# Kernel optimization log

Hardware: AMD Instinct MI355X
Metric: run time of the kernel (lower is better)

The kernel has to match this reference:

```python
import jax, jax.numpy as jnp
import numpy as np
import math

HEADS = 16
DIMS = 1024
SEQ_LEN = 2048
RANK_K = 128
BATCH = 8


def setup_inputs() -> dict:
    key = jax.random.key(0)
    ks = jax.random.split(key, 14)
    dh_std = 1.0 / math.sqrt(DIMS)
    proj_std = 1.0 / math.sqrt(RANK_K)
    inp = {
        "q": jax.random.normal(ks[0], (BATCH, SEQ_LEN, DIMS), jnp.float32),
        "k": jax.random.normal(ks[1], (BATCH, SEQ_LEN, DIMS), jnp.float32),
        "v": jax.random.normal(ks[2], (BATCH, SEQ_LEN, DIMS), jnp.float32),
        # nn.Linear weights [out, in], bias [out]
        "Wq": jax.random.uniform(ks[3], (DIMS, DIMS), jnp.float32, -dh_std, dh_std),
        "bq": jax.random.uniform(ks[4], (DIMS,), jnp.float32, -dh_std, dh_std),
        "Wk": jax.random.uniform(ks[5], (DIMS, DIMS), jnp.float32, -dh_std, dh_std),
        "bk": jax.random.uniform(ks[6], (DIMS,), jnp.float32, -dh_std, dh_std),
        "Wv": jax.random.uniform(ks[7], (DIMS, DIMS), jnp.float32, -dh_std, dh_std),
        "bv": jax.random.uniform(ks[8], (DIMS,), jnp.float32, -dh_std, dh_std),
        # Linformer low-rank projections [seq_length, k], uniform(-1/sqrt(k), 1/sqrt(k))
        "proj_k": jax.random.uniform(ks[9], (SEQ_LEN, RANK_K), jnp.float32, -proj_std, proj_std),
        "proj_v": jax.random.uniform(ks[10], (SEQ_LEN, RANK_K), jnp.float32, -proj_std, proj_std),
        "Wo": jax.random.uniform(ks[11], (DIMS, DIMS), jnp.float32, -dh_std, dh_std),
        "bo": jax.random.uniform(ks[12], (DIMS,), jnp.float32, -dh_std, dh_std),
    }
    return inp


def reference(q, k, v, Wq, bq, Wk, bk, Wv, bv, proj_k, proj_v, Wo, bo):
    B, N, D = q.shape
    H = HEADS
    dh = D // H
    Kr = proj_k.shape[1]

    kp = k @ Wk.T + bk                       # [B, N, D]
    # faithful to original: plain reshape (view), NOT a head-split transpose
    qp = (q @ Wq.T + bq).reshape(B, H, N, dh)  # [B, H, N, dh]
    vp = v @ Wv.T + bv                       # [B, N, D]

    pk = jnp.einsum('bnd,nk->bkd', kp, proj_k[:N])  # [B, Kr, D]
    pv = jnp.einsum('bnd,nk->bkd', vp, proj_v[:N])  # [B, Kr, D]
    pk = pk.reshape(B, Kr, H, dh).transpose(0, 2, 1, 3)  # [B, H, Kr, dh]
    pv = pv.reshape(B, Kr, H, dh).transpose(0, 2, 1, 3)  # [B, H, Kr, dh]

    # scores [B,H,N,Kr] -> transposed to [B,H,Kr,N]; softmax over N (seq) axis
    scores = jnp.einsum('bhnd,bhkd->bhkn', qp, pk) / math.sqrt(dh)
    attn = jax.nn.softmax(scores, axis=-1)   # [B, H, Kr, N]
    out = jnp.einsum('bhkn,bhkd->bhnd', attn, pv)  # [B, H, N, dh]
    out = out.transpose(0, 2, 1, 3).reshape(B, N, D)
    return out @ Wo.T + bo
```

## Files before the change

kernel.cpp:

```cpp
#include <hip/hip_runtime.h>

typedef unsigned short u16;
typedef unsigned int   u32;
typedef __attribute__((ext_vector_type(4))) float fx4;
typedef __attribute__((ext_vector_type(8))) __bf16 bf16x8;
typedef __attribute__((ext_vector_type(4))) __bf16 bf16x4;
typedef __attribute__((ext_vector_type(8))) unsigned short us8;
typedef __attribute__((ext_vector_type(2))) unsigned int u32x2;

__device__ __forceinline__ u16 f2bf(float x){
  u32 u = __builtin_bit_cast(u32, x);
  u += 0x7fffu + ((u >> 16) & 1u);
  return (u16)(u >> 16);
}
__device__ __forceinline__ float b2f(u16 h){
  u32 u = ((u32)h) << 16;
  return __builtin_bit_cast(float, u);
}
__device__ __forceinline__ void gld16(const void* g, void* l){
  __builtin_amdgcn_global_load_lds(
      (const __attribute__((address_space(1))) u32*)g,
      (__attribute__((address_space(3))) u32*)l, 16, 0, 0);
}
__device__ __forceinline__ void xcd_remap(u32& bx, u32& by, u32& bz){
  u32 nx = gridDim.x, ny = gridDim.y, nz = gridDim.z;
  u32 nwg = nx * ny * nz;
  u32 orig = (blockIdx.z * ny + blockIdx.y) * nx + blockIdx.x;
  u32 lid = (orig & 7u) * (nwg >> 3) + (orig >> 3);
  bx = lid % nx;
  u32 rem = lid / nx;
  by = rem % ny;
  bz = rem / ny;
}

__global__ __launch_bounds__(256) void k_f2bfAll(const float* __restrict__ w0,
                                                 const float* __restrict__ w1,
                                                 const float* __restrict__ w2,
                                                 const float* __restrict__ w3,
                                                 const float* __restrict__ q,
                                                 u16* __restrict__ wout,
                                                 u16* __restrict__ qout,
                                                 float* __restrict__ zbuf){
  if (blockIdx.x == 0 && blockIdx.y == 0) zbuf[threadIdx.x] = 0.f;
  const int y = blockIdx.y;
  const float* src;
  u16* dst;
  if (y < 4){
    src = y == 0 ? w0 : y == 1 ? w1 : y == 2 ? w2 : w3;
    dst = wout + (long)y * 1048576;
  } else {
    src = q + (long)(y - 4) * 1048576;
    dst = qout + (long)(y - 4) * 1048576;
  }
  int i = blockIdx.x * 256 + threadIdx.x;
  const int stride = gridDim.x * 256;
  for (; i < 131072; i += stride){
    const float4* p = (const float4*)src + (long)i * 2;
    float4 a = p[0], b = p[1];
    us8 o = { f2bf(a.x), f2bf(a.y), f2bf(a.z), f2bf(a.w),
              f2bf(b.x), f2bf(b.y), f2bf(b.z), f2bf(b.w) };
    *((us8*)dst + i) = o;
  }
}

__global__ __launch_bounds__(256) void k_tconvP(const float* __restrict__ pjk,
                                                const float* __restrict__ pjv,
                                                u16* __restrict__ projT,
                                                float* __restrict__ ssum){
  const int z = blockIdx.z;
  const float* in = z ? pjv : pjk;
  u16* out = projT + z * 262144;
  float* colsum = ssum + z * 128;
  const int c0 = blockIdx.x * 64, r0 = blockIdx.y * 64;
  __shared__ u16 tile[64][66];
  __shared__ float red[256];
  const int t = threadIdx.x;
  const int cc = t & 63, wq = t >> 6;
  float part = 0.f;
  #pragma unroll
  for (int i = 0; i < 16; ++i){
    int rr = i * 4 + wq;
    float v = in[(long)(r0 + rr) * 128 + c0 + cc];
    tile[rr][cc] = f2bf(v);
    part += v;
  }
  red[t] = part;
  __syncthreads();
  if (t < 64){
    float s = red[t] + red[t + 64] + red[t + 128] + red[t + 192];
    atomicAdd(&colsum[c0 + t], s);
  }
  __syncthreads();
  const int oc0 = t >> 5, jb = (t & 31) * 2;
  #pragma unroll
  for (int i = 0; i < 8; ++i){
    int oc = oc0 + i * 8;
    u32 pk2 = (u32)tile[jb][oc] | ((u32)tile[jb + 1][oc] << 16);
    *(u32*)(out + (long)(c0 + oc) * 2048 + r0 + jb) = pk2;
  }
}

__global__ __launch_bounds__(256) void k_gemmTN(
    const u16* __restrict__ projT, const float* __restrict__ ksrc,
    const float* __restrict__ vsrc, u16* __restrict__ ck)
{
  u32 bx, by, bz; xcd_remap(bx, by, bz);
  const int p = bz >> 3, b = bz & 7;
  const u16* A = projT + p * 262144 + by * 64 * 2048;
  const float* S = (p ? vsrc : ksrc) + (long)b * 2097152;
  u16* C = ck + p * 1048576 + b * 131072 + by * 65536;
  const int d0 = bx * 64;
  __shared__ u16 ldsA[3][64 * 64];
  __shared__ u16 ldsB[3][64 * 72];
  const int t = threadIdx.x, lane = t & 63, w = t >> 6;
  const int wm = w >> 1, wn = w & 1;
  const int r15 = lane & 15, g = lane >> 4;
  const int c4 = t & 15, r4 = t >> 4;

  auto ldA = [&](int kt, int buf){
    #pragma unroll
    for (int i = 0; i < 2; ++i){
      int ch = i * 256 + t, row = ch >> 3, cc = ch & 7;
      gld16(A + (long)row * 2048 + kt + ((cc ^ (row & 7)) * 8),
            (char*)ldsA[buf] + ch * 16);
    }
  };
  auto ldS = [&](int kt, float4* f){
    #pragma unroll
    for (int i = 0; i < 4; ++i)
      f[i] = *(const float4*)(S + (long)(kt + r4 * 4 + i) * 1024 + d0 + c4 * 4);
  };
  auto wrB = [&](const float4* f, int buf){
    #pragma unroll
    for (int j = 0; j < 4; ++j){
      const int d = c4 * 4 + j;
      u32 lo = (u32)f2bf(((const float*)&f[0])[j]) | ((u32)f2bf(((const float*)&f[1])[j]) << 16);
      u32 hi = (u32)f2bf(((const float*)&f[2])[j]) | ((u32)f2bf(((const float*)&f[3])[j]) << 16);
      u32x2 pr = { lo, hi };
      *(u32x2*)&ldsB[buf][d * 72 + ((r4 ^ (d & 15)) * 4)] = pr;
    }
  };

  fx4 acc[2][2] = {};
  auto compute = [&](int buf){
    #pragma unroll
    for (int ks = 0; ks < 2; ++ks){
      bf16x8 af[2], bfv[2];
      #pragma unroll
      for (int mf = 0; mf < 2; ++mf){
        int row = wm * 32 + mf * 16 + r15;
        af[mf] = *(const bf16x8*)((const char*)ldsA[buf] + row * 128 +
                                  (((ks * 4 + g) ^ (row & 7)) * 16));
      }
      #pragma unroll
      for (int nf = 0; nf < 2; ++nf){
        const int d = wn * 32 + nf * 16 + r15, x = d & 15;
        const int q0 = ks * 8 + g * 2;
        bf16x4 lo = *(const bf16x4*)&ldsB[buf][d * 72 + ((q0 ^ x) * 4)];
        bf16x4 hi = *(const bf16x4*)&ldsB[buf][d * 72 + (((q0 + 1) ^ x) * 4)];
        bfv[nf] = __builtin_shufflevector(lo, hi, 0, 1, 2, 3, 4, 5, 6, 7);
      }
      #pragma unroll
      for (int mf = 0; mf < 2; ++mf)
        #pragma unroll
        for (int nf = 0; nf < 2; ++nf)
          acc[mf][nf] = __builtin_amdgcn_mfma_f32_16x16x32_bf16(af[mf], bfv[nf], acc[mf][nf], 0, 0, 0);
    }
  };

  float4 fa[4], fb[4];
  ldS(0, fa); ldA(0, 0);
  ldS(64, fb); ldA(64, 1);
  asm volatile("s_waitcnt vmcnt(6)" ::: "memory");
  wrB(fa, 0);
  asm volatile("s_waitcnt lgkmcnt(0)" ::: "memory");
  __builtin_amdgcn_s_barrier();
  asm volatile("" ::: "memory");

  for (int tt = 0; tt < 32; tt += 2){
    {
      const bool pf = (tt + 2 < 32);
      if (pf){ ldS((tt + 2) * 64, fa); ldA((tt + 2) * 64, (tt + 2) % 3); }
      asm volatile("" ::: "memory");
      compute(tt % 3);
      if (pf) { asm volatile("s_waitcnt vmcnt(6)" ::: "memory"); }
      else    { asm volatile("s_waitcnt vmcnt(0)" ::: "memory"); }
      wrB(fb, (tt + 1) % 3);
      asm volatile("s_waitcnt lgkmcnt(0)" ::: "memory");
      __builtin_amdgcn_s_barrier();
      asm volatile("" ::: "memory");
    }
    {
      const bool pf = (tt + 3 < 32);
      const bool hv = (tt + 2 < 32);
      if (pf){ ldS((tt + 3) * 64, fb); ldA((tt + 3) * 64, (tt + 3) % 3); }
      asm volatile("" ::: "memory");
      compute((tt + 1) % 3);
      if (hv){
        if (pf) { asm volatile("s_waitcnt vmcnt(6)" ::: "memory"); }
        else    { asm volatile("s_waitcnt vmcnt(0)" ::: "memory"); }
        wrB(fa, (tt + 2) % 3);
      }
      asm volatile("s_waitcnt lgkmcnt(0)" ::: "memory");
      __builtin_amdgcn_s_barrier();
      asm volatile("" ::: "memory");
    }
  }

  #pragma unroll
  for (int mf = 0; mf < 2; ++mf)
    #pragma unroll
    for (int nf = 0; nf < 2; ++nf){
      const int row0 = wm * 32 + mf * 16 + g * 4;
      const int col  = d0 + wn * 32 + nf * 16 + r15;
      #pragma unroll
      for (int r = 0; r < 4; ++r)
        C[(long)(row0 + r) * 1024 + col] = f2bf(acc[mf][nf][r]);
    }
}

__global__ __launch_bounds__(256) void k_pkpv(
    const u16* __restrict__ ck, const u16* __restrict__ Wk_bf,
    const u16* __restrict__ Wv_bf, const float* __restrict__ bk,
    const float* __restrict__ bv, const float* __restrict__ ssum,
    u16* __restrict__ pk, u16* __restrict__ pvT)
{
  constexpr int BM = 64, BN = 64, BK = 64;
  __shared__ u16 ldsA[BM * BK];
  __shared__ u16 ldsB[BN * BK];
  u32 bx, by, bz;
  xcd_remap(bx, by, bz);
  const int half = bz >> 3, b = bz & 7;
  const u16* A = ck + half * 1048576 + b * 131072;
  const u16* B = half ? Wv_bf : Wk_bf;
  const float* bias = half ? bv : bk;
  const float* srow = ssum + half * 128;
  const float scale = half ? 1.f : 0.125f;
  const int t = threadIdx.x;
  const int lane = t & 63;
  const int w = t >> 6, wm = w >> 1, wn = w & 1;
  const int r15 = lane & 15, g = lane >> 4;
  const int m0 = by * BM, n0 = bx * BN;
  fx4 acc[2][2] = {};
  for (int kt = 0; kt < 1024; kt += BK){
    #pragma unroll
    for (int i = 0; i < 2; ++i){
      int ch = i * 256 + t, row = ch >> 3, cc = ch & 7;
      gld16(A + (long)(m0 + row) * 1024 + kt + cc * 8, (char*)ldsA + ch * 16);
    }
    #pragma unroll
    for (int i = 0; i < 2; ++i){
      int ch = i * 256 + t, row = ch >> 3, cc = ch & 7;
      gld16(B + (long)(n0 + row) * 1024 + kt + cc * 8, (char*)ldsB + ch * 16);
    }
    __syncthreads();
    #pragma unroll
    for (int ks = 0; ks < 2; ++ks){
      bf16x8 af[2], bfv[2];
      #pragma unroll
      for (int mf = 0; mf < 2; ++mf)
        af[mf] = *(const bf16x8*)&ldsA[(wm * 32 + mf * 16 + r15) * BK + ks * 32 + g * 8];
      #pragma unroll
      for (int nf = 0; nf < 2; ++nf)
        bfv[nf] = *(const bf16x8*)&ldsB[(wn * 32 + nf * 16 + r15) * BK + ks * 32 + g * 8];
      #pragma unroll
      for (int mf = 0; mf < 2; ++mf)
        #pragma unroll
        for (int nf = 0; nf < 2; ++nf)
          acc[mf][nf] = __builtin_amdgcn_mfma_f32_16x16x32_bf16(af[mf], bfv[nf], acc[mf][nf], 0, 0, 0);
    }
    __syncthreads();
  }
  #pragma unroll
  for (int mf = 0; mf < 2; ++mf){
    #pragma unroll
    for (int nf = 0; nf < 2; ++nf){
      const int row0 = m0 + wm * 32 + mf * 16 + g * 4;
      const int col  = n0 + wn * 32 + nf * 16 + r15;
      float vv[4];
      #pragma unroll
      for (int r = 0; r < 4; ++r)
        vv[r] = (acc[mf][nf][r] + srow[row0 + r] * bias[col]) * scale;
      if (!half){
        #pragma unroll
        for (int r = 0; r < 4; ++r)
          pk[b * 131072 + (long)(row0 + r) * 1024 + col] = f2bf(vv[r]);
      } else {
        u32 lo = (u32)f2bf(vv[0]) | ((u32)f2bf(vv[1]) << 16);
        u32 hi = (u32)f2bf(vv[2]) | ((u32)f2bf(vv[3]) << 16);
        u32x2 pk2 = { lo, hi };
        *(u32x2*)(pvT + b * 131072 + (long)col * 128 + row0) = pk2;
      }
    }
  }
}

template<int EPI, typename OutT>
__global__ __launch_bounds__(512, 1) void k_gemm256b(
    const u16* __restrict__ A, int lda,
    const u16* __restrict__ B, int ldb,
    OutT* __restrict__ C, int ldc,
    int K, const float* __restrict__ bias)
{
  constexpr int BM = 256, BN = 256, BK = 64;
  __shared__ u16 ldsA[2][BM * BK];
  __shared__ u16 ldsB[2][BN * BK];
  u32 bx, by, bz;
  xcd_remap(bx, by, bz);
  const int m0 = by * BM, n0 = bx * BN;
  const int t = threadIdx.x, lane = t & 63, w = t >> 6;
  const int wm = w >> 2, wn = w & 3;
  const int r15 = lane & 15, g = lane >> 4;
  const int NT = K >> 6;

  auto stA = [&](int buf, int half, int kt){
    #pragma unroll
    for (int j = 0; j < 2; ++j){
      int ch = j * 512 + t, row = ch >> 3, cc = ch & 7;
      gld16(A + (long)(m0 + half * 128 + row) * lda + kt + ((cc ^ (row & 7)) * 8),
            (char*)ldsA[buf] + half * 16384 + ch * 16);
    }
  };
  auto stB = [&](int buf, int half, int kt){
    #pragma unroll
    for (int j = 0; j < 2; ++j){
      int ch = j * 512 + t, row = ch >> 3, cc = ch & 7;
      gld16(B + (long)(n0 + half * 128 + row) * ldb + kt + ((cc ^ (row & 7)) * 8),
            (char*)ldsB[buf] + half * 16384 + ch * 16);
    }
  };

  stB(0,0,0); stB(0,1,0); stA(0,0,0); stA(0,1,0);
  if (NT > 1){ stB(1,0,BK); stB(1,1,BK); stA(1,0,BK); }
  asm volatile("s_waitcnt vmcnt(6)" ::: "memory");
  __builtin_amdgcn_s_barrier();
  asm volatile("" ::: "memory");

  fx4 acc[8][4] = {};
  for (int tt = 0; tt < NT; ++tt){
    const int buf = tt & 1;
    bf16x8 a[2][4], b01[2][2], b23[2][2];
    #pragma unroll
    for (int ks = 0; ks < 2; ++ks)
      #pragma unroll
      for (int mf = 0; mf < 4; ++mf){
        int row = wm * 128 + mf * 16 + r15;
        a[ks][mf] = *(const bf16x8*)((const char*)ldsA[buf] + row * 128 + (((ks*4+g) ^ (r15 & 7)) * 16));
      }
    #pragma unroll
    for (int ks = 0; ks < 2; ++ks)
      #pragma unroll
      for (int nf = 0; nf < 2; ++nf){
        int row = wn * 64 + nf * 16 + r15;
        b01[ks][nf] = *(const bf16x8*)((const char*)ldsB[buf] + row * 128 + (((ks*4+g) ^ (r15 & 7)) * 16));
      }
    if (tt + 1 < NT) stA(buf ^ 1, 1, (tt + 1) * BK);
    __builtin_amdgcn_s_setprio(1);
    #pragma unroll
    for (int ks = 0; ks < 2; ++ks)
      #pragma unroll
      for (int mf = 0; mf < 4; ++mf)
        #pragma unroll
        for (int nf = 0; nf < 2; ++nf)
          acc[mf][nf] = __builtin_amdgcn_mfma_f32_16x16x32_bf16(a[ks][mf], b01[ks][nf], acc[mf][nf], 0, 0, 0);
    __builtin_amdgcn_s_setprio(0);
    asm volatile("" ::: "memory");
    __builtin_amdgcn_s_barrier();
    asm volatile("" ::: "memory");
    #pragma unroll
    for (int ks = 0; ks < 2; ++ks)
      #pragma unroll
      for (int nf = 0; nf < 2; ++nf){
        int row = wn * 64 + (nf + 2) * 16 + r15;
        b23[ks][nf] = *(const bf16x8*)((const char*)ldsB[buf] + row * 128 + (((ks*4+g) ^ (r15 & 7)) * 16));
      }
    __builtin_amdgcn_s_setprio(1);
    #pragma unroll
    for (int ks = 0; ks < 2; ++ks)
      #pragma unroll
      for (int mf = 0; mf < 4; ++mf)
        #pragma unroll
        for (int nf = 0; nf < 2; ++nf)
          acc[mf][nf + 2] = __builtin_amdgcn_mfma_f32_16x16x32_bf16(a[ks][mf], b23[ks][nf], acc[mf][nf + 2], 0, 0, 0);
    __builtin_amdgcn_s_setprio(0);
    asm volatile("" ::: "memory");
    __builtin_amdgcn_s_barrier();
    asm volatile("" ::: "memory");
    #pragma unroll
    for (int ks = 0; ks < 2; ++ks)
      #pragma unroll
      for (int mf = 0; mf < 4; ++mf){
        int row = wm * 128 + (mf + 4) * 16 + r15;
        a[ks][mf] = *(const bf16x8*)((const char*)ldsA[buf] + row * 128 + (((ks*4+g) ^ (r15 & 7)) * 16));
      }
    if (tt + 2 < NT) stB(buf, 0, (tt + 2) * BK);
    __builtin_amdgcn_s_setprio(1);
    #pragma unroll
    for (int ks = 0; ks < 2; ++ks)
      #pragma unroll
      for (int mf = 0; mf < 4; ++mf)
        #pragma unroll
        for (int nf = 0; nf < 2; ++nf)
          acc[mf + 4][nf + 2] = __builtin_amdgcn_mfma_f32_16x16x32_bf16(a[ks][mf], b23[ks][nf], acc[mf + 4][nf + 2], 0, 0, 0);
    __builtin_amdgcn_s_setprio(0);
    asm volatile("" ::: "memory");
    __builtin_amdgcn_s_barrier();
    asm volatile("" ::: "memory");
    if (tt + 2 < NT){ stA(buf, 0, (tt + 2) * BK); stB(buf, 1, (tt + 2) * BK); }
    __builtin_amdgcn_s_setprio(1);
    #pragma unroll
    for (int ks = 0; ks < 2; ++ks)
      #pragma unroll
      for (int mf = 0; mf < 4; ++mf)
        #pragma unroll
        for (int nf = 0; nf < 2; ++nf)
          acc[mf + 4][nf] = __builtin_amdgcn_mfma_f32_16x16x32_bf16(a[ks][mf], b01[ks][nf], acc[mf + 4][nf], 0, 0, 0);
    __builtin_amdgcn_s_setprio(0);
    if (tt + 2 < NT)      { asm volatile("s_waitcnt vmcnt(6)" ::: "memory"); }
    else if (tt + 1 < NT) { asm volatile("s_waitcnt vmcnt(0)" ::: "memory"); }
    asm volatile("" ::: "memory");
    __builtin_amdgcn_s_barrier();
    asm volatile("" ::: "memory");
  }

  #pragma unroll
  for (int mf = 0; mf < 8; ++mf)
    #pragma unroll
    for (int nf = 0; nf < 4; ++nf){
      const int row0 = m0 + wm * 128 + mf * 16 + g * 4;
      const int col  = n0 + wn * 64 + nf * 16 + r15;
      float bcol = 0.f;
      if constexpr (EPI == 1) bcol = bias[col];
      #pragma unroll
      for (int r = 0; r < 4; ++r){
        float vv = acc[mf][nf][r] + bcol;
        if constexpr (sizeof(OutT) == 2) C[(long)(row0 + r) * ldc + col] = (OutT)f2bf(vv);
        else                             C[(long)(row0 + r) * ldc + col] = (OutT)vv;
      }
    }
}

__global__ __launch_bounds__(512) void k_stats(const u16* __restrict__ pk,
                                               const u16* __restrict__ qp,
                                               float* __restrict__ zpart){
  const int hf = blockIdx.x, z = blockIdx.y;
  const int b = z >> 4, h = z & 15;
  const u16* pkh = pk + b * 131072 + h * 64;
  const u16* qph = qp + (long)z * 131072;
  __shared__ u16 pkL[128 * 64];
  __shared__ float zred[8][128];
  const int t = threadIdx.x, lane = t & 63, w = t >> 6;
  const int r15 = lane & 15, g = lane >> 4;
  #pragma unroll
  for (int i = 0; i < 2; ++i){
    int ch = i * 512 + t, row = ch >> 3, cc = ch & 7;
    int csrc = cc ^ (row & 7);
    gld16(pkh + (long)row * 1024 + csrc * 8, (char*)pkL + ch * 16);
  }
  __syncthreads();
  float zacc[8][4] = {};
  for (int c = 0; c < 4; ++c){
    const int n0 = hf * 1024 + w * 128 + c * 32;
    fx4 acc[8][2] = {};
    #pragma unroll
    for (int ks = 0; ks < 2; ++ks){
      bf16x8 bq[2];
      #pragma unroll
      for (int nf = 0; nf < 2; ++nf)
        bq[nf] = *(const bf16x8*)(qph + (long)(n0 + nf * 16 + r15) * 64 + ks * 32 + g * 8);
      #pragma unroll
      for (int mf = 0; mf < 8; ++mf){
        int row = mf * 16 + r15;
        int x = (ks * 4 + g) ^ (row & 7);
        bf16x8 a = *(const bf16x8*)((const char*)pkL + row * 128 + x * 16);
        #pragma unroll
        for (int nf = 0; nf < 2; ++nf)
          acc[mf][nf] = __builtin_amdgcn_mfma_f32_16x16x32_bf16(a, bq[nf], acc[mf][nf], 0, 0, 0);
      }
    }
    #pragma unroll
    for (int mf = 0; mf < 8; ++mf)
      #pragma unroll
      for (int nf = 0; nf < 2; ++nf)
        #pragma unroll
        for (int r = 0; r < 4; ++r)
          zacc[mf][r] += __expf(acc[mf][nf][r]);
  }
  #pragma unroll
  for (int mf = 0; mf < 8; ++mf)
    #pragma unroll
    for (int r = 0; r < 4; ++r){
      float v = zacc[mf][r];
      v += __shfl_xor(v, 1); v += __shfl_xor(v, 2);
      v += __shfl_xor(v, 4); v += __shfl_xor(v, 8);
      zacc[mf][r] = v;
    }
  if (r15 == 0){
    #pragma unroll
    for (int mf = 0; mf < 8; ++mf)
      #pragma unroll
      for (int r = 0; r < 4; ++r)
        zred[w][mf * 16 + g * 4 + r] = zacc[mf][r];
  }
  __syncthreads();
  if (t < 128){
    float s = 0.f;
    #pragma unroll
    for (int w2 = 0; w2 < 8; ++w2) s += zred[w2][t];
    zpart[hf * 16384 + (long)z * 128 + t] = s;
  }
}

__global__ __launch_bounds__(256) void k_attn(const u16* __restrict__ pk,
                                              const u16* __restrict__ qp,
                                              const u16* __restrict__ pvT,
                                              const float* __restrict__ zpart,
                                              u16* __restrict__ outh){
  u32 bx, by, bz;
  xcd_remap(bx, by, bz);
  const int z = by, nb = bx;
  const int b = z >> 4, h = z & 15;
  const u16* pkh = pk  + b * 131072 + h * 64;
  const u16* qph = qp  + (long)z * 131072;
  const u16* pvh = pvT + b * 131072 + h * 8192;
  __shared__ u16 pkL[128 * 64];
  __shared__ u16 ptL[4][32 * 132];
  __shared__ float zL[128];
  const int t = threadIdx.x, lane = t & 63, w = t >> 6;
  const int r15 = lane & 15, g = lane >> 4;
  #pragma unroll
  for (int i = 0; i < 4; ++i){
    int ch = i * 256 + t, row = ch >> 3, cc = ch & 7;
    int csrc = cc ^ (row & 7);
    gld16(pkh + (long)row * 1024 + csrc * 8, (char*)pkL + ch * 16);
  }
  if (t < 128)
    zL[t] = 1.0f / (zpart[(long)z * 128 + t] + zpart[16384 + (long)z * 128 + t]);
  __syncthreads();
  const int n0 = nb * 128 + w * 32;
  fx4 acc[8][2] = {};
  #pragma unroll
  for (int ks = 0; ks < 2; ++ks){
    bf16x8 bq[2];
    #pragma unroll
    for (int nf = 0; nf < 2; ++nf)
      bq[nf] = *(const bf16x8*)(qph + (long)(n0 + nf * 16 + r15) * 64 + ks * 32 + g * 8);
    #pragma unroll
    for (int mf = 0; mf < 8; ++mf){
      int row = mf * 16 + r15;
      int x = (ks * 4 + g) ^ (row & 7);
      bf16x8 a = *(const bf16x8*)((const char*)pkL + row * 128 + x * 16);
      #pragma unroll
      for (int nf = 0; nf < 2; ++nf)
        acc[mf][nf] = __builtin_amdgcn_mfma_f32_16x16x32_bf16(a, bq[nf], acc[mf][nf], 0, 0, 0);
    }
  }
  u16* pt = ptL[w];
  #pragma unroll
  for (int mf = 0; mf < 8; ++mf){
    const int kb = mf * 16 + g * 4;
    const float z0 = zL[kb], z1 = zL[kb + 1], z2 = zL[kb + 2], z3 = zL[kb + 3];
    #pragma unroll
    for (int nf = 0; nf < 2; ++nf){
      const int nl = nf * 16 + r15;
      u32 lo = (u32)f2bf(__expf(acc[mf][nf][0]) * z0) |
               ((u32)f2bf(__expf(acc[mf][nf][1]) * z1) << 16);
      u32 hi = (u32)f2bf(__expf(acc[mf][nf][2]) * z2) |
               ((u32)f2bf(__expf(acc[mf][nf][3]) * z3) << 16);
      u32x2 pkd = { lo, hi };
      *(u32x2*)(pt + nl * 132 + kb) = pkd;
    }
  }
  fx4 o[2][4] = {};
  #pragma unroll
  for (int ks = 0; ks < 4; ++ks){
    bf16x8 bv[4];
    #pragma unroll
    for (int nf = 0; nf < 4; ++nf)
      bv[nf] = *(const bf16x8*)(pvh + (long)(nf * 16 + r15) * 128 + ks * 32 + g * 8);
    #pragma unroll
    for (int mf = 0; mf < 2; ++mf){
      bf16x8 pa = *(const bf16x8*)(pt + (mf * 16 + r15) * 132 + ks * 32 + g * 8);
      #pragma unroll
      for (int nf = 0; nf < 4; ++nf)
        o[mf][nf] = __builtin_amdgcn_mfma_f32_16x16x32_bf16(pa, bv[nf], o[mf][nf], 0, 0, 0);
    }
  }
  u16* og = outh + ((long)b * 2048 + n0) * 1024 + h * 64;
  #pragma unroll
  for (int mf = 0; mf < 2; ++mf)
    #pragma unroll
    for (int nf = 0; nf < 4; ++nf)
      #pragma unroll
      for (int r = 0; r < 4; ++r){
        int nl = mf * 16 + g * 4 + r;
        og[(long)nl * 1024 + nf * 16 + r15] = f2bf(o[mf][nf][r]);
      }
}

extern "C" void kernel_launch(void* const* d_in, const int* in_sizes, int n_in,
                              void* d_out, int out_size, void* d_ws, size_t ws_size,
                              hipStream_t stream)
{
  const float* q   = (const float*)d_in[0];
  const float* k   = (const float*)d_in[1];
  const float* v   = (const float*)d_in[2];
  const float* Wq  = (const float*)d_in[3];
  const float* bq  = (const float*)d_in[4];
  const float* Wk  = (const float*)d_in[5];
  const float* bk  = (const float*)d_in[6];
  const float* Wv  = (const float*)d_in[7];
  const float* bv  = (const float*)d_in[8];
  const float* pjk = (const float*)d_in[9];
  const float* pjv = (const float*)d_in[10];
  const float* Wo  = (const float*)d_in[11];
  const float* bo  = (const float*)d_in[12];

  if (ws_size < 152044544u) return;

  char* ws = (char*)d_ws;
  u16*  q_bf  = (u16*)(ws + 0);
  float* zpart = (float*)(ws + 33554432);
  u16*  W_bf  = (u16*)(ws + 100663296);
  u16*  projT = (u16*)(ws + 109051904);
  float* sk   = (float*)(ws + 110100480);
  u16*  qp    = (u16*)(ws + 110101504);
  u16*  ck    = (u16*)(ws + 143655936);
  u16*  pk    = (u16*)(ws + 147850240);
  u16*  pvT   = (u16*)(ws + 149947392);
  u16*  outh  = (u16*)(ws + 0);
  u16*  Wq_bf = W_bf, *Wk_bf = W_bf + 1048576, *Wv_bf = W_bf + 2097152, *Wo_bf = W_bf + 3145728;

  k_f2bfAll<<<dim3(128,20), 256, 0, stream>>>(Wq, Wk, Wv, Wo, q, W_bf, q_bf, sk);
  k_tconvP<<<dim3(2,32,2), 256, 0, stream>>>(pjk, pjv, projT, sk);

  k_gemm256b<1,u16><<<dim3(4,64), 512, 0, stream>>>(
      q_bf,1024, Wq_bf,1024, qp,1024, 1024, bq);
  k_gemmTN<<<dim3(16,2,16), 256, 0, stream>>>(projT, k, v, ck);
  k_pkpv<<<dim3(16,2,16), 256, 0, stream>>>(ck, Wk_bf, Wv_bf, bk, bv, sk, pk, pvT);
  k_stats<<<dim3(2,128), 512, 0, stream>>>(pk, qp, zpart);
  k_attn<<<dim3(16,128), 256, 0, stream>>>(pk, qp, pvT, zpart, outh);
  k_gemm256b<1,float><<<dim3(4,64), 512, 0, stream>>>(
      outh,1024, Wo_bf,1024, (float*)d_out,1024, 1024, bo);
}
```

Before: 221.7 us.

## Split gemmTN sequence reduction in two halves and sum partials in pkpv

Result: slower. 229.7 us (+3.6%).

```diff
diff --git a/kernel.cpp b/kernel.cpp
--- a/kernel.cpp
+++ b/kernel.cpp
@@ -102,13 +102,14 @@
 
 __global__ __launch_bounds__(256) void k_gemmTN(
     const u16* __restrict__ projT, const float* __restrict__ ksrc,
-    const float* __restrict__ vsrc, u16* __restrict__ ck)
+    const float* __restrict__ vsrc, u16* __restrict__ ckA,
+    u16* __restrict__ ckB)
 {
   u32 bx, by, bz; xcd_remap(bx, by, bz);
-  const int p = bz >> 3, b = bz & 7;
-  const u16* A = projT + p * 262144 + by * 64 * 2048;
-  const float* S = (p ? vsrc : ksrc) + (long)b * 2097152;
-  u16* C = ck + p * 1048576 + b * 131072 + by * 65536;
+  const int half = bz >> 4, p = (bz >> 3) & 1, b = bz & 7;
+  const u16* A = projT + p * 262144 + by * 64 * 2048 + half * 1024;
+  const float* S = (p ? vsrc : ksrc) + (long)b * 2097152 + (long)half * 1048576;
+  u16* C = (half ? ckB : ckA) + p * 1048576 + b * 131072 + by * 65536;
   const int d0 = bx * 64;
   __shared__ u16 ldsA[3][64 * 64];
   __shared__ u16 ldsB[3][64 * 72];
@@ -168,6 +169,7 @@
     }
   };
 
+  constexpr int NT = 16;
   float4 fa[4], fb[4];
   ldS(0, fa); ldA(0, 0);
   ldS(64, fb); ldA(64, 1);
@@ -177,9 +179,9 @@
   __builtin_amdgcn_s_barrier();
   asm volatile("" ::: "memory");
 
-  for (int tt = 0; tt < 32; tt += 2){
+  for (int tt = 0; tt < NT; tt += 2){
     {
-      const bool pf = (tt + 2 < 32);
+      const bool pf = (tt + 2 < NT);
       if (pf){ ldS((tt + 2) * 64, fa); ldA((tt + 2) * 64, (tt + 2) % 3); }
       asm volatile("" ::: "memory");
       compute(tt % 3);
@@ -191,8 +193,8 @@
       asm volatile("" ::: "memory");
     }
     {
-      const bool pf = (tt + 3 < 32);
-      const bool hv = (tt + 2 < 32);
+      const bool pf = (tt + 3 < NT);
+      const bool hv = (tt + 2 < NT);
       if (pf){ ldS((tt + 3) * 64, fb); ldA((tt + 3) * 64, (tt + 3) % 3); }
       asm volatile("" ::: "memory");
       compute((tt + 1) % 3);
@@ -220,9 +222,10 @@
 }
 
 __global__ __launch_bounds__(256) void k_pkpv(
-    const u16* __restrict__ ck, const u16* __restrict__ Wk_bf,
-    const u16* __restrict__ Wv_bf, const float* __restrict__ bk,
-    const float* __restrict__ bv, const float* __restrict__ ssum,
+    const u16* __restrict__ ckA, const u16* __restrict__ ckB,
+    const u16* __restrict__ Wk_bf, const u16* __restrict__ Wv_bf,
+    const float* __restrict__ bk, const float* __restrict__ bv,
+    const float* __restrict__ ssum,
     u16* __restrict__ pk, u16* __restrict__ pvT)
 {
   constexpr int BM = 64, BN = 64, BK = 64;
@@ -230,46 +233,50 @@
   __shared__ u16 ldsB[BN * BK];
   u32 bx, by, bz;
   xcd_remap(bx, by, bz);
-  const int half = bz >> 3, b = bz & 7;
-  const u16* A = ck + half * 1048576 + b * 131072;
-  const u16* B = half ? Wv_bf : Wk_bf;
-  const float* bias = half ? bv : bk;
-  const float* srow = ssum + half * 128;
-  const float scale = half ? 1.f : 0.125f;
+  const int hv = bz >> 3, b = bz & 7;
+  const long aoff = hv * 1048576 + b * 131072;
+  const u16* B = hv ? Wv_bf : Wk_bf;
+  const float* bias = hv ? bv : bk;
+  const float* srow = ssum + hv * 128;
+  const float scale = hv ? 1.f : 0.125f;
   const int t = threadIdx.x;
   const int lane = t & 63;
   const int w = t >> 6, wm = w >> 1, wn = w & 1;
   const int r15 = lane & 15, g = lane >> 4;
   const int m0 = by * BM, n0 = bx * BN;
   fx4 acc[2][2] = {};
-  for (int kt = 0; kt < 1024; kt += BK){
-    #pragma unroll
-    for (int i = 0; i < 2; ++i){
-      int ch = i * 256 + t, row = ch >> 3, cc = ch & 7;
-      gld16(A + (long)(m0 + row) * 1024 + kt + cc * 8, (char*)ldsA + ch * 16);
-    }
-    #pragma unroll
-    for (int i = 0; i < 2; ++i){
-      int ch = i * 256 + t, row = ch >> 3, cc = ch & 7;
-      gld16(B + (long)(n0 + row) * 1024 + kt + cc * 8, (char*)ldsB + ch * 16);
-    }
-    __syncthreads();
-    #pragma unroll
-    for (int ks = 0; ks < 2; ++ks){
-      bf16x8 af[2], bfv[2];
-      #pragma unroll
-      for (int mf = 0; mf < 2; ++mf)
-        af[mf] = *(const bf16x8*)&ldsA[(wm * 32 + mf * 16 + r15) * BK + ks * 32 + g * 8];
-      #pragma unroll
-      for (int nf = 0; nf < 2; ++nf)
-        bfv[nf] = *(const bf16x8*)&ldsB[(wn * 32 + nf * 16 + r15) * BK + ks * 32 + g * 8];
-      #pragma unroll
-      for (int mf = 0; mf < 2; ++mf)
+  #pragma unroll 1
+  for (int src = 0; src < 2; ++src){
+    const u16* A = (src ? ckB : ckA) + aoff;
+    for (int kt = 0; kt < 1024; kt += BK){
+      #pragma unroll
+      for (int i = 0; i < 2; ++i){
+        int ch = i * 256 + t, row = ch >> 3, cc = ch & 7;
+        gld16(A + (long)(m0 + row) * 1024 + kt + cc * 8, (char*)ldsA + ch * 16);
+      }
+      #pragma unroll
+      for (int i = 0; i < 2; ++i){
+        int ch = i * 256 + t, row = ch >> 3, cc = ch & 7;
+        gld16(B + (long)(n0 + row) * 1024 + kt + cc * 8, (char*)ldsB + ch * 16);
+      }
+      __syncthreads();
+      #pragma unroll
+      for (int ks = 0; ks < 2; ++ks){
+        bf16x8 af[2], bfv[2];
+        #pragma unroll
+        for (int mf = 0; mf < 2; ++mf)
+          af[mf] = *(const bf16x8*)&ldsA[(wm * 32 + mf * 16 + r15) * BK + ks * 32 + g * 8];
         #pragma unroll
         for (int nf = 0; nf < 2; ++nf)
-          acc[mf][nf] = __builtin_amdgcn_mfma_f32_16x16x32_bf16(af[mf], bfv[nf], acc[mf][nf], 0, 0, 0);
-    }
-    __syncthreads();
+          bfv[nf] = *(const bf16x8*)&ldsB[(wn * 32 + nf * 16 + r15) * BK + ks * 32 + g * 8];
+        #pragma unroll
+        for (int mf = 0; mf < 2; ++mf)
+          #pragma unroll
+          for (int nf = 0; nf < 2; ++nf)
+            acc[mf][nf] = __builtin_amdgcn_mfma_f32_16x16x32_bf16(af[mf], bfv[nf], acc[mf][nf], 0, 0, 0);
+      }
+      __syncthreads();
+    }
   }
   #pragma unroll
   for (int mf = 0; mf < 2; ++mf){
@@ -281,7 +288,7 @@
       #pragma unroll
       for (int r = 0; r < 4; ++r)
         vv[r] = (acc[mf][nf][r] + srow[row0 + r] * bias[col]) * scale;
-      if (!half){
+      if (!hv){
         #pragma unroll
         for (int r = 0; r < 4; ++r)
           pk[b * 131072 + (long)(row0 + r) * 1024 + col] = f2bf(vv[r]);
@@ -621,11 +628,12 @@
   char* ws = (char*)d_ws;
   u16*  q_bf  = (u16*)(ws + 0);
   float* zpart = (float*)(ws + 33554432);
+  u16*  ckB   = (u16*)(ws + 41943040);
   u16*  W_bf  = (u16*)(ws + 100663296);
   u16*  projT = (u16*)(ws + 109051904);
   float* sk   = (float*)(ws + 110100480);
   u16*  qp    = (u16*)(ws + 110101504);
-  u16*  ck    = (u16*)(ws + 143655936);
+  u16*  ckA   = (u16*)(ws + 143655936);
   u16*  pk    = (u16*)(ws + 147850240);
   u16*  pvT   = (u16*)(ws + 149947392);
   u16*  outh  = (u16*)(ws + 0);
@@ -636,8 +644,8 @@
 
   k_gemm256b<1,u16><<<dim3(4,64), 512, 0, stream>>>(
       q_bf,1024, Wq_bf,1024, qp,1024, 1024, bq);
-  k_gemmTN<<<dim3(16,2,16), 256, 0, stream>>>(projT, k, v, ck);
-  k_pkpv<<<dim3(16,2,16), 256, 0, stream>>>(ck, Wk_bf, Wv_bf, bk, bv, sk, pk, pvT);
+  k_gemmTN<<<dim3(16,2,32), 256, 0, stream>>>(projT, k, v, ckA, ckB);
+  k_pkpv<<<dim3(16,2,16), 256, 0, stream>>>(ckA, ckB, Wk_bf, Wv_bf, bk, bv, sk, pk, pvT);
   k_stats<<<dim3(2,128), 512, 0, stream>>>(pk, qp, zpart);
   k_attn<<<dim3(16,128), 256, 0, stream>>>(pk, qp, pvT, zpart, outh);
   k_gemm256b<1,float><<<dim3(4,64), 512, 0, stream>>>(
```
